# Performance work log

Measured on AMD Instinct MI355X. Metric: run time of the kernel, lower is better.

## Reference

```python
import jax, jax.numpy as jnp
import numpy as np

D_MODEL = 1024
H = 16
HEAD = D_MODEL // H  # 64


def setup_inputs() -> dict:
    key = jax.random.key(0)
    ks = jax.random.split(key, 10)
    B, S = 2, 2048
    x = jax.random.normal(ks[0], (B, S, D_MODEL), dtype=jnp.float32)
    y = jax.random.normal(ks[1], (B, S, D_MODEL), dtype=jnp.float32)
    mask = jnp.ones((B, S, S), dtype=jnp.float32)
    s = 1.0 / np.sqrt(D_MODEL)
    Wq = jax.random.normal(ks[2], (D_MODEL, D_MODEL), dtype=jnp.float32) * s
    Wk = jax.random.normal(ks[3], (D_MODEL, D_MODEL), dtype=jnp.float32) * s
    Wv = jax.random.normal(ks[4], (D_MODEL, D_MODEL), dtype=jnp.float32) * s
    Wo = jax.random.normal(ks[5], (D_MODEL, D_MODEL), dtype=jnp.float32) * s
    bq = jnp.zeros((D_MODEL,), jnp.float32)
    bk = jnp.zeros((D_MODEL,), jnp.float32)
    bv = jnp.zeros((D_MODEL,), jnp.float32)
    bo = jnp.zeros((D_MODEL,), jnp.float32)
    return {"x": x, "y": y, "mask": mask, "Wq": Wq, "bq": bq, "Wk": Wk,
            "bk": bk, "Wv": Wv, "bv": bv, "Wo": Wo, "bo": bo}


def reference(x, y, mask, Wq, bq, Wk, bk, Wv, bv, Wo, bo):
    # torch Linear: out = in @ W.T + b; here W stored as [out, in]
    B, Sq, D = x.shape
    Skv = y.shape[1]
    q = x @ Wq.T + bq  # [B, Sq, D]
    k = y @ Wk.T + bk  # [B, Skv, D]
    v = y @ Wv.T + bv
    # chunk(h, dim=-1) + cat(dim=0) == split feature dim into heads (head-major)
    q = q.reshape(B, Sq, H, HEAD)
    k = k.reshape(B, Skv, H, HEAD)
    v = v.reshape(B, Skv, H, HEAD)
    score = jnp.einsum('bqhd,bkhd->bhqk', q, k) / np.sqrt(HEAD)
    score = score + (1.0 - mask[:, None, :, :]) * -1e9
    attn = jax.nn.softmax(score, axis=-1)
    out = jnp.einsum('bhqk,bkhd->bqhd', attn, v).reshape(B, Sq, D)
    return out @ Wo.T + bo
```

## Files before the change

### kernel.cpp

```cpp
#include <hip/hip_runtime.h>
#include <cstdint>
#include <cstddef>

typedef __bf16 bf16x8 __attribute__((ext_vector_type(8)));
typedef float f32x4 __attribute__((ext_vector_type(4)));
typedef unsigned short u16;
typedef unsigned short u16x8 __attribute__((ext_vector_type(8)));
typedef unsigned int u32;

typedef __attribute__((address_space(1))) void gvoid_t;
typedef __attribute__((address_space(3))) void lvoid_t;

__device__ __forceinline__ void gld_lds16(const void* g, void* l) {
  __builtin_amdgcn_global_load_lds((gvoid_t*)g, (lvoid_t*)l, 16, 0, 0);
}

__device__ __forceinline__ u16 f2bf(float f) {
  u32 u = __float_as_uint(f);
  u += 0x7fffu + ((u >> 16) & 1u);
  return (u16)(u >> 16);
}
__device__ __forceinline__ u32 pack_rnd(float a, float b) {
  const u32 ua = __float_as_uint(a) + 0x8000u;
  const u32 ub = __float_as_uint(b) + 0x8000u;
  return __builtin_amdgcn_perm(ub, ua, 0x07060302u);
}
__device__ __forceinline__ bf16x8 ld_frag(const u16* p) {
  return __builtin_bit_cast(bf16x8, *(const uint4*)p);
}
__device__ __forceinline__ f32x4 mfma16(bf16x8 a, bf16x8 b, f32x4 c) {
  return __builtin_amdgcn_mfma_f32_16x16x32_bf16(a, b, c, 0, 0, 0);
}
__device__ __forceinline__ float ex2(float x) {
  return __builtin_amdgcn_exp2f(x);
}

#define D_MODEL 1024
#define SEQ     2048
#define NHEAD   16
#define QSC     0.1803368801f
#define MBIAS   (-1.4426950408e9f)

__global__ __launch_bounds__(256) void pre_kernel(
    const float* __restrict__ x,  const float* __restrict__ y,
    const float* __restrict__ wq, const float* __restrict__ wk,
    const float* __restrict__ wv,
    u16* __restrict__ xb, u16* __restrict__ yb,
    u16* __restrict__ wqb, u16* __restrict__ wkb,
    u16* __restrict__ wvb) {
  const int bid = blockIdx.x;
  const float* src;
  u16* dst;
  int base;
  float sA = 1.0f;
  if (bid < 2048)      { src = x;    dst = xb;    base = 0; }
  else if (bid < 4096) { src = y;    dst = yb;    base = 2048; }
  else if (bid < 4608) { src = wq;   dst = wqb;   base = 4096; sA = QSC; }
  else if (bid < 5120) { src = wk;   dst = wkb;   base = 4608; }
  else                 { src = wv;   dst = wvb;   base = 5120; }
  const int i = (((bid - base) * 256) + threadIdx.x) * 8;
  const float4 a = *(const float4*)(src + i);
  const float4 b = *(const float4*)(src + i + 4);
  ushort4 lo, hi;
  lo.x = f2bf(a.x * sA); lo.y = f2bf(a.y * sA);
  lo.z = f2bf(a.z * sA); lo.w = f2bf(a.w * sA);
  hi.x = f2bf(b.x * sA); hi.y = f2bf(b.y * sA);
  hi.z = f2bf(b.z * sA); hi.w = f2bf(b.w * sA);
  *(ushort4*)(dst + i) = lo;
  *(ushort4*)(dst + i + 4) = hi;
}

template <int MODE, typename OT>
__device__ __forceinline__ void gemm_block_128(u16* S,
                                               const u16* __restrict__ A,
                                               const u16* __restrict__ W,
                                               const float* __restrict__ bias,
                                               float bscale,
                                               OT* __restrict__ D,
                                               int mb, int nb) {
  u16* Asl = S;
  u16* Bsl = S + 8192;
  const int tid = threadIdx.x;
  const int w = tid >> 6, lane = tid & 63, quad = lane >> 4, l16 = lane & 15;
  const int wm = (w & 1) * 64, wn = (w >> 1) * 64;
  const int cidx = w * 64 + lane;

  f32x4 acc[4][4];
#pragma unroll
  for (int i = 0; i < 4; ++i)
#pragma unroll
    for (int j = 0; j < 4; ++j) acc[i][j] = f32x4{0.f, 0.f, 0.f, 0.f};

  for (int k0 = 0; k0 < 1024; k0 += 64) {
    __syncthreads();
#pragma unroll
    for (int t = 0; t < 4; ++t) {
      const int idx = t * 256 + cidx;
      const int row = idx >> 3;
      const int g = (idx & 7) ^ (row & 7);
      const size_t dst = (size_t)(t * 4 + w) * 1024;
      gld_lds16(A + (size_t)(mb * 128 + row) * 1024 + k0 + g * 8, (char*)Asl + dst);
      gld_lds16(W + (size_t)(nb * 128 + row) * 1024 + k0 + g * 8, (char*)Bsl + dst);
    }
    __syncthreads();

#pragma unroll
    for (int kk = 0; kk < 2; ++kk) {
      bf16x8 af[4], bfr[4];
#pragma unroll
      for (int i = 0; i < 4; ++i) {
        const int ar = wm + i * 16 + l16;
        const int br = wn + i * 16 + l16;
        af[i]  = ld_frag(Asl + ar * 64 + (((kk * 4 + quad) ^ (ar & 7)) * 8));
        bfr[i] = ld_frag(Bsl + br * 64 + (((kk * 4 + quad) ^ (br & 7)) * 8));
      }
#pragma unroll
      for (int i = 0; i < 4; ++i)
#pragma unroll
        for (int j = 0; j < 4; ++j) acc[i][j] = mfma16(af[i], bfr[j], acc[i][j]);
    }
  }

  if constexpr (MODE == 2) {
    __syncthreads();
#pragma unroll
    for (int i = 0; i < 4; ++i)
#pragma unroll
      for (int j = 0; j < 4; ++j) {
        const int dl = wn + j * 16 + l16;
        const float bv = bias[nb * 128 + dl];
        const int sx = (wm + i * 16 + quad * 4) ^ ((dl & 15) << 3);
        uint2 pv;
        pv.x = (u32)f2bf(acc[i][j][0] + bv) | ((u32)f2bf(acc[i][j][1] + bv) << 16);
        pv.y = (u32)f2bf(acc[i][j][2] + bv) | ((u32)f2bf(acc[i][j][3] + bv) << 16);
        *(uint2*)(S + dl * 128 + sx) = pv;
      }
    __syncthreads();
    const int dl = tid >> 1, half = tid & 1;
    const int bb = mb >> 4, s0 = (mb & 15) * 128;
    u16* vrow = (u16*)D + (size_t)(bb * 1024 + nb * 128 + dl) * SEQ + s0 + half * 64;
#pragma unroll
    for (int c = 0; c < 8; ++c) {
      const int pc = (half * 8 + c) ^ (dl & 15);
      *(uint4*)(vrow + c * 8) = *(const uint4*)(S + dl * 128 + pc * 8);
    }
  } else {
#pragma unroll
    for (int i = 0; i < 4; ++i)
#pragma unroll
      for (int j = 0; j < 4; ++j) {
        const int gn = nb * 128 + wn + j * 16 + l16;
        const float bv = bias[gn] * bscale;
#pragma unroll
        for (int r = 0; r < 4; ++r) {
          const int gm = mb * 128 + wm + i * 16 + quad * 4 + r;
          const float v = acc[i][j][r] + bv;
          if constexpr (sizeof(OT) == 2)
            D[(size_t)gm * 1024 + gn] = (OT)f2bf(v);
          else
            D[(size_t)gm * 1024 + gn] = (OT)v;
        }
      }
  }
}

__device__ __forceinline__ void gemm_block_n64(const u16* __restrict__ A,
                                               const u16* __restrict__ W,
                                               const float* __restrict__ bias,
                                               float* __restrict__ D,
                                               int mb, int nb) {
  __shared__ __align__(16) u16 S[12288];
  u16* Asl = S;
  u16* Bsl = S + 8192;
  const int tid = threadIdx.x;
  const int w = tid >> 6, lane = tid & 63, quad = lane >> 4, l16 = lane & 15;
  const int wm = w * 32;
  const int cidx = w * 64 + lane;

  f32x4 acc[2][4];
#pragma unroll
  for (int i = 0; i < 2; ++i)
#pragma unroll
    for (int j = 0; j < 4; ++j) acc[i][j] = f32x4{0.f, 0.f, 0.f, 0.f};

  for (int k0 = 0; k0 < 1024; k0 += 64) {
    __syncthreads();
#pragma unroll
    for (int t = 0; t < 4; ++t) {
      const int idx = t * 256 + cidx;
      const int row = idx >> 3;
      const int g = (idx & 7) ^ (row & 7);
      gld_lds16(A + (size_t)(mb * 128 + row) * 1024 + k0 + g * 8,
                (char*)Asl + (size_t)(t * 4 + w) * 1024);
    }
#pragma unroll
    for (int t = 0; t < 2; ++t) {
      const int idx = t * 256 + cidx;
      const int row = idx >> 3;
      const int g = (idx & 7) ^ (row & 7);
      gld_lds16(W + (size_t)(nb * 64 + row) * 1024 + k0 + g * 8,
                (char*)Bsl + (size_t)(t * 4 + w) * 1024);
    }
    __syncthreads();

#pragma unroll
    for (int kk = 0; kk < 2; ++kk) {
      bf16x8 af[2], bfr[4];
#pragma unroll
      for (int i = 0; i < 2; ++i) {
        const int ar = wm + i * 16 + l16;
        af[i] = ld_frag(Asl + ar * 64 + (((kk * 4 + quad) ^ (ar & 7)) * 8));
      }
#pragma unroll
      for (int j = 0; j < 4; ++j) {
        const int br = j * 16 + l16;
        bfr[j] = ld_frag(Bsl + br * 64 + (((kk * 4 + quad) ^ (br & 7)) * 8));
      }
#pragma unroll
      for (int i = 0; i < 2; ++i)
#pragma unroll
        for (int j = 0; j < 4; ++j) acc[i][j] = mfma16(af[i], bfr[j], acc[i][j]);
    }
  }

#pragma unroll
  for (int i = 0; i < 2; ++i)
#pragma unroll
    for (int j = 0; j < 4; ++j) {
      const int gn = nb * 64 + j * 16 + l16;
      const float bv = bias[gn];
#pragma unroll
      for (int r = 0; r < 4; ++r) {
        const int gm = mb * 128 + wm + i * 16 + quad * 4 + r;
        D[(size_t)gm * 1024 + gn] = acc[i][j][r] + bv;
      }
    }
}

__global__ __launch_bounds__(256) void qkv_kernel(
    const u16* __restrict__ xb, const u16* __restrict__ yb,
    const u16* __restrict__ Wqb, const u16* __restrict__ Wkb, const u16* __restrict__ Wvb,
    const float* __restrict__ bq, const float* __restrict__ bk, const float* __restrict__ bv,
    const float* __restrict__ mask, const float* __restrict__ wo,
    u16* __restrict__ qb, u16* __restrict__ kb, u16* __restrict__ vt,
    u16* __restrict__ wob, u32* __restrict__ flags) {
  __shared__ __align__(16) u16 S[16384];
  const int by = blockIdx.y;
  if (by < 4) {
    const int mx = by * 32 + blockIdx.x;
    const int lane = threadIdx.x & 63, wv8 = threadIdx.x >> 6;
    for (int r = 0; r < 32; ++r) {
      const int row = mx * 32 + r;
      const size_t i = (size_t)row * SEQ + threadIdx.x * 8;
      const float4 a = *(const float4*)(mask + i);
      const float4 b = *(const float4*)(mask + i + 4);
      const bool m8 = (a.x != 1.f) || (a.y != 1.f) || (a.z != 1.f) || (a.w != 1.f) ||
                      (b.x != 1.f) || (b.y != 1.f) || (b.z != 1.f) || (b.w != 1.f);
      const unsigned long long bal = __ballot(m8);
      if (lane == 0) {
        u32 bits = 0;
#pragma unroll
        for (int g = 0; g < 8; ++g)
          bits |= (((bal >> (8 * g)) & 0xFFull) ? 1u : 0u) << g;
        if (bits) {
          const int bb = row >> 11, q = row & 2047;
          atomicOr(&flags[bb * 32 + (q >> 6)], bits << (wv8 * 8));
        }
      }
    }
    return;
  }
  if (by < 20) {
    const int wid = (by - 4) * 32 + blockIdx.x;
    const int i = (wid * 256 + threadIdx.x) * 8;
    const float4 a = *(const float4*)(wo + i);
    const float4 b = *(const float4*)(wo + i + 4);
    ushort4 lo, hi;
    lo.x = f2bf(a.x); lo.y = f2bf(a.y); lo.z = f2bf(a.z); lo.w = f2bf(a.w);
    hi.x = f2bf(b.x); hi.y = f2bf(b.y); hi.z = f2bf(b.z); hi.w = f2bf(b.w);
    *(ushort4*)(wob + i) = lo;
    *(ushort4*)(wob + i + 4) = hi;
    return;
  }
  const int mat = (by - 20) >> 3;
  const int nb = (by - 20) & 7;
  const int mb = blockIdx.x;
  if (mat == 0)      gemm_block_128<0, u16>(S, xb, Wqb, bq, QSC,  qb, mb, nb);
  else if (mat == 1) gemm_block_128<0, u16>(S, yb, Wkb, bk, 1.0f, kb, mb, nb);
  else               gemm_block_128<2, u16>(S, yb, Wvb, bv, 1.0f, vt, mb, nb);
}

__global__ __launch_bounds__(256) void oproj_kernel(
    const u16* __restrict__ ctx, const u16* __restrict__ Wob,
    const float* __restrict__ bo, float* __restrict__ out) {
  gemm_block_n64(ctx, Wob, bo, out, blockIdx.x, blockIdx.y);
}

__global__ __launch_bounds__(256, 4) void attn_kernel(
    const u16* __restrict__ qb, const u16* __restrict__ kb,
    const u16* __restrict__ vt, const float* __restrict__ mask,
    const u32* __restrict__ flags, u16* __restrict__ ctx) {
  const int h = blockIdx.x;
  const int qblk = blockIdx.y;
  const int b = blockIdx.z;
  const int tid = threadIdx.x, w = tid >> 6, lane = tid & 63;
  const int quad = lane >> 4, l16 = lane & 15;
  const int q0 = qblk * 64;

  __shared__ __align__(16) u16 Ks[64 * 64];
  __shared__ __align__(16) u16 Vs[64 * 64];
  __shared__ __align__(16) u16 Ps[64 * 64];

  const u32 fl = flags[(b << 5) + qblk];

  const int qrow = w * 16 + l16;
  const u16* qp = qb + (size_t)(b * SEQ + q0 + qrow) * D_MODEL + h * 64;
  const bf16x8 qf0 = ld_frag(qp + quad * 8);
  const bf16x8 qf1 = ld_frag(qp + 32 + quad * 8);

  bf16x8 onesf;
  {
    u16x8 t;
    const u16 ov = (l16 == 0) ? (u16)0x3F80 : (u16)0;
#pragma unroll
    for (int j = 0; j < 8; ++j) t[j] = ov;
    onesf = __builtin_bit_cast(bf16x8, t);
  }

  f32x4 O[4];
#pragma unroll
  for (int dt = 0; dt < 4; ++dt) O[dt] = f32x4{0.f, 0.f, 0.f, 0.f};
  f32x4 O4 = f32x4{0.f, 0.f, 0.f, 0.f};

  const int cidx = w * 64 + lane;
  const int bhalf = (quad & 1) * 4;

  const u16 *kf0p[4], *kf1p[4], *vf0p[4], *vf1p[4];
  u16* psp[4];
#pragma unroll
  for (int nt = 0; nt < 4; ++nt) {
    const int rl = nt * 16 + l16;
    kf0p[nt] = Ks + rl * 64 + ((quad ^ (rl & 7)) * 8);
    kf1p[nt] = Ks + rl * 64 + (((4 + quad) ^ (rl & 7)) * 8);
    vf0p[nt] = Vs + rl * 64 + ((quad ^ (rl & 7)) * 8);
    vf1p[nt] = Vs + rl * 64 + (((4 + quad) ^ (rl & 7)) * 8);
    const int ck = nt * 2 + (quad >> 1);
    psp[nt] = Ps + qrow * 64 + ((ck ^ (qrow & 7)) * 8) + bhalf;
  }
  const u16* pf0p = Ps + qrow * 64 + ((quad ^ (qrow & 7)) * 8);
  const u16* pf1p = Ps + qrow * 64 + (((4 + quad) ^ (qrow & 7)) * 8);

  const int r0 = cidx >> 3,        g0 = (cidx & 7) ^ (r0 & 7);
  const int r1 = (256 + cidx) >> 3, g1 = ((256 + cidx) & 7) ^ (r1 & 7);
  const u16* kp0 = kb + (size_t)(b * SEQ + r0) * D_MODEL + h * 64 + g0 * 8;
  const u16* kp1 = kb + (size_t)(b * SEQ + r1) * D_MODEL + h * 64 + g1 * 8;
  const u16* vp0 = vt + ((size_t)((b * NHEAD + h) * 64 + r0)) * SEQ + g0 * 8;
  const u16* vp1 = vt + ((size_t)((b * NHEAD + h) * 64 + r1)) * SEQ + g1 * 8;
  const float* mp = mask + (size_t)(b * SEQ + q0 + qrow) * SEQ + quad * 4;
  const size_t dst0 = (size_t)w * 1024;
  const size_t dst1 = (size_t)(4 + w) * 1024;

  for (int kt = 0; kt < 32; ++kt) {
    const bool doBias = (fl >> kt) & 1u;
    __syncthreads();
    gld_lds16(kp0, (char*)Ks + dst0);
    gld_lds16(kp1, (char*)Ks + dst1);
    gld_lds16(vp0, (char*)Vs + dst0);
    gld_lds16(vp1, (char*)Vs + dst1);
    kp0 += 64 * D_MODEL; kp1 += 64 * D_MODEL;
    vp0 += 64;           vp1 += 64;
    __syncthreads();

    f32x4 z[4];
    __builtin_amdgcn_s_setprio(1);
#pragma unroll
    for (int nt = 0; nt < 4; ++nt) {
      const bf16x8 kf0 = ld_frag(kf0p[nt]);
      const bf16x8 kf1 = ld_frag(kf1p[nt]);
      f32x4 zz;
      if (doBias) {
        const float4 mv = *(const float4*)(mp + nt * 16);
        zz[0] = (1.f - mv.x) * MBIAS;
        zz[1] = (1.f - mv.y) * MBIAS;
        zz[2] = (1.f - mv.z) * MBIAS;
        zz[3] = (1.f - mv.w) * MBIAS;
      } else {
        zz = f32x4{0.f, 0.f, 0.f, 0.f};
      }
      zz = mfma16(kf0, qf0, zz);
      zz = mfma16(kf1, qf1, zz);
      z[nt] = zz;
    }
    __builtin_amdgcn_s_setprio(0);
    mp += 64;
#pragma unroll
    for (int nt = 0; nt < 4; ++nt) {
      uint2 pv;
      pv.x = pack_rnd(ex2(z[nt][0]), ex2(z[nt][1]));
      pv.y = pack_rnd(ex2(z[nt][2]), ex2(z[nt][3]));
      *(uint2*)psp[nt] = pv;
    }

    const bf16x8 pf0 = ld_frag(pf0p);
    const bf16x8 pf1 = ld_frag(pf1p);
    __builtin_amdgcn_s_setprio(1);
#pragma unroll
    for (int dt = 0; dt < 4; ++dt) {
      const bf16x8 vf0 = ld_frag(vf0p[dt]);
      const bf16x8 vf1 = ld_frag(vf1p[dt]);
      O[dt] = mfma16(pf0, vf0, O[dt]);
      O[dt] = mfma16(pf1, vf1, O[dt]);
    }
    O4 = mfma16(pf0, onesf, O4);
    O4 = mfma16(pf1, onesf, O4);
    __builtin_amdgcn_s_setprio(0);
  }

  float inv[4];
#pragma unroll
  for (int r = 0; r < 4; ++r)
    inv[r] = 1.0f / __shfl(O4[r], lane & 48, 64);

#pragma unroll
  for (int dt = 0; dt < 4; ++dt)
#pragma unroll
    for (int r = 0; r < 4; ++r) {
      const int gq = b * SEQ + q0 + w * 16 + quad * 4 + r;
      const int gd = h * 64 + dt * 16 + l16;
      ctx[(size_t)gq * D_MODEL + gd] = f2bf(O[dt][r] * inv[r]);
    }
}

extern "C" void kernel_launch(void* const* d_in, const int* in_sizes, int n_in,
                              void* d_out, int out_size, void* d_ws, size_t ws_size,
                              hipStream_t stream) {
  (void)in_sizes; (void)n_in; (void)out_size; (void)ws_size;
  const float* x    = (const float*)d_in[0];
  const float* y    = (const float*)d_in[1];
  const float* mask = (const float*)d_in[2];
  const float* Wq   = (const float*)d_in[3];
  const float* bq   = (const float*)d_in[4];
  const float* Wk   = (const float*)d_in[5];
  const float* bk   = (const float*)d_in[6];
  const float* Wv   = (const float*)d_in[7];
  const float* bv   = (const float*)d_in[8];
  const float* Wo   = (const float*)d_in[9];
  const float* bo   = (const float*)d_in[10];
  float* out = (float*)d_out;

  const size_t M4 = (size_t)4096 * 1024;
  const size_t M1 = (size_t)1024 * 1024;
  u16* qbuf  = (u16*)d_ws;
  u16* kbuf  = qbuf + M4;
  u16* vt    = kbuf + M4;
  u16* cbuf  = vt + M4;
  u16* wob   = cbuf + M4;
  u16* xb    = wob + M1;
  u16* yb    = xb + M4;
  u16* wqb   = yb + M4;
  u16* wkb   = wqb + M1;
  u16* wvb   = wkb + M1;
  u32* flags = (u32*)(wvb + M1);

  hipMemsetAsync(flags, 0, 64 * sizeof(u32), stream);
  pre_kernel<<<dim3(5632, 1, 1), 256, 0, stream>>>(
      x, y, Wq, Wk, Wv, xb, yb, wqb, wkb, wvb);
  qkv_kernel<<<dim3(32, 44, 1), 256, 0, stream>>>(xb, yb, wqb, wkb, wvb,
                                                  bq, bk, bv, mask, Wo,
                                                  qbuf, kbuf, vt, wob, flags);
  attn_kernel<<<dim3(NHEAD, 32, 2), 256, 0, stream>>>(qbuf, kbuf, vt, mask, flags, cbuf);
  oproj_kernel<<<dim3(32, 16, 1), 256, 0, stream>>>(cbuf, wob, bo, out);
}
```

Measured before the change: 238.9 us.

## Split attention warps 2x2 over query and key halves with LDS reduction

Changes the per-block warp work split in the attention kernel. Before, each of the four warps owned 16 query rows across all 64 keys. Now the warps form a 2x2 grid: each owns 32 query rows and half of the key tile, so each K and V fragment loaded from LDS is reused across two query subtiles. The per-warp partial O and row sums are combined at the end through LDS. This adds a final barrier, more registers per thread, and an epilogue where half the warps sit idle.

```diff
diff --git a/kernel.cpp b/kernel.cpp
--- a/kernel.cpp
+++ b/kernel.cpp
@@ -305,6 +305,7 @@
   const int b = blockIdx.z;
   const int tid = threadIdx.x, w = tid >> 6, lane = tid & 63;
   const int quad = lane >> 4, l16 = lane & 15;
+  const int qg = w & 1, kg = w >> 1;
   const int q0 = qblk * 64;
 
   __shared__ __align__(16) u16 Ks[64 * 64];
@@ -313,10 +314,14 @@
 
   const u32 fl = flags[(b << 5) + qblk];
 
-  const int qrow = w * 16 + l16;
-  const u16* qp = qb + (size_t)(b * SEQ + q0 + qrow) * D_MODEL + h * 64;
-  const bf16x8 qf0 = ld_frag(qp + quad * 8);
-  const bf16x8 qf1 = ld_frag(qp + 32 + quad * 8);
+  bf16x8 qf[2][2];
+#pragma unroll
+  for (int qs = 0; qs < 2; ++qs) {
+    const int qrow = qg * 32 + qs * 16 + l16;
+    const u16* qp = qb + (size_t)(b * SEQ + q0 + qrow) * D_MODEL + h * 64;
+    qf[qs][0] = ld_frag(qp + quad * 8);
+    qf[qs][1] = ld_frag(qp + 32 + quad * 8);
+  }
 
   bf16x8 onesf;
   {
@@ -327,28 +332,39 @@
     onesf = __builtin_bit_cast(bf16x8, t);
   }
 
-  f32x4 O[4];
-#pragma unroll
-  for (int dt = 0; dt < 4; ++dt) O[dt] = f32x4{0.f, 0.f, 0.f, 0.f};
-  f32x4 O4 = f32x4{0.f, 0.f, 0.f, 0.f};
+  f32x4 O[4][2];
+#pragma unroll
+  for (int dt = 0; dt < 4; ++dt)
+#pragma unroll
+    for (int qs = 0; qs < 2; ++qs) O[dt][qs] = f32x4{0.f, 0.f, 0.f, 0.f};
+  f32x4 L[2] = {f32x4{0.f, 0.f, 0.f, 0.f}, f32x4{0.f, 0.f, 0.f, 0.f}};
 
   const int cidx = w * 64 + lane;
   const int bhalf = (quad & 1) * 4;
 
-  const u16 *kf0p[4], *kf1p[4], *vf0p[4], *vf1p[4];
-  u16* psp[4];
-#pragma unroll
-  for (int nt = 0; nt < 4; ++nt) {
-    const int rl = nt * 16 + l16;
-    kf0p[nt] = Ks + rl * 64 + ((quad ^ (rl & 7)) * 8);
-    kf1p[nt] = Ks + rl * 64 + (((4 + quad) ^ (rl & 7)) * 8);
-    vf0p[nt] = Vs + rl * 64 + ((quad ^ (rl & 7)) * 8);
-    vf1p[nt] = Vs + rl * 64 + (((4 + quad) ^ (rl & 7)) * 8);
-    const int ck = nt * 2 + (quad >> 1);
-    psp[nt] = Ps + qrow * 64 + ((ck ^ (qrow & 7)) * 8) + bhalf;
-  }
-  const u16* pf0p = Ps + qrow * 64 + ((quad ^ (qrow & 7)) * 8);
-  const u16* pf1p = Ps + qrow * 64 + (((4 + quad) ^ (qrow & 7)) * 8);
+  const u16 *kf0p[2], *kf1p[2], *vfp[4], *pfp[2];
+  u16* psp[2][2];
+#pragma unroll
+  for (int nt = 0; nt < 2; ++nt) {
+    const int kvl = kg * 32 + nt * 16 + l16;
+    kf0p[nt] = Ks + kvl * 64 + ((quad ^ (kvl & 7)) * 8);
+    kf1p[nt] = Ks + kvl * 64 + (((4 + quad) ^ (kvl & 7)) * 8);
+  }
+#pragma unroll
+  for (int dt = 0; dt < 4; ++dt) {
+    const int vr = dt * 16 + l16;
+    vfp[dt] = Vs + vr * 64 + ((((kg * 4) + quad) ^ (vr & 7)) * 8);
+  }
+#pragma unroll
+  for (int qs = 0; qs < 2; ++qs) {
+    const int prow = qg * 32 + qs * 16 + l16;
+    pfp[qs] = Ps + prow * 64 + ((((kg * 4) + quad) ^ (prow & 7)) * 8);
+#pragma unroll
+    for (int nt = 0; nt < 2; ++nt) {
+      const int ck = kg * 4 + nt * 2 + (quad >> 1);
+      psp[qs][nt] = Ps + prow * 64 + ((ck ^ (prow & 7)) * 8) + bhalf;
+    }
+  }
 
   const int r0 = cidx >> 3,        g0 = (cidx & 7) ^ (r0 & 7);
   const int r1 = (256 + cidx) >> 3, g1 = ((256 + cidx) & 7) ^ (r1 & 7);
@@ -356,7 +372,11 @@
   const u16* kp1 = kb + (size_t)(b * SEQ + r1) * D_MODEL + h * 64 + g1 * 8;
   const u16* vp0 = vt + ((size_t)((b * NHEAD + h) * 64 + r0)) * SEQ + g0 * 8;
   const u16* vp1 = vt + ((size_t)((b * NHEAD + h) * 64 + r1)) * SEQ + g1 * 8;
-  const float* mp = mask + (size_t)(b * SEQ + q0 + qrow) * SEQ + quad * 4;
+  const float* mp[2];
+#pragma unroll
+  for (int qs = 0; qs < 2; ++qs)
+    mp[qs] = mask + (size_t)(b * SEQ + q0 + qg * 32 + qs * 16 + l16) * SEQ
+                  + kg * 32 + quad * 4;
   const size_t dst0 = (size_t)w * 1024;
   const size_t dst1 = (size_t)(4 + w) * 1024;
 
@@ -371,64 +391,102 @@
     vp0 += 64;           vp1 += 64;
     __syncthreads();
 
-    f32x4 z[4];
+    f32x4 z[2][2];
     __builtin_amdgcn_s_setprio(1);
 #pragma unroll
-    for (int nt = 0; nt < 4; ++nt) {
+    for (int nt = 0; nt < 2; ++nt) {
       const bf16x8 kf0 = ld_frag(kf0p[nt]);
       const bf16x8 kf1 = ld_frag(kf1p[nt]);
-      f32x4 zz;
-      if (doBias) {
-        const float4 mv = *(const float4*)(mp + nt * 16);
-        zz[0] = (1.f - mv.x) * MBIAS;
-        zz[1] = (1.f - mv.y) * MBIAS;
-        zz[2] = (1.f - mv.z) * MBIAS;
-        zz[3] = (1.f - mv.w) * MBIAS;
-      } else {
-        zz = f32x4{0.f, 0.f, 0.f, 0.f};
-      }
-      zz = mfma16(kf0, qf0, zz);
-      zz = mfma16(kf1, qf1, zz);
-      z[nt] = zz;
+#pragma unroll
+      for (int qs = 0; qs < 2; ++qs) {
+        f32x4 zz;
+        if (doBias) {
+          const float4 mv = *(const float4*)(mp[qs] + nt * 16);
+          zz[0] = (1.f - mv.x) * MBIAS;
+          zz[1] = (1.f - mv.y) * MBIAS;
+          zz[2] = (1.f - mv.z) * MBIAS;
+          zz[3] = (1.f - mv.w) * MBIAS;
+        } else {
+          zz = f32x4{0.f, 0.f, 0.f, 0.f};
+        }
+        zz = mfma16(kf0, qf[qs][0], zz);
+        zz = mfma16(kf1, qf[qs][1], zz);
+        z[nt][qs] = zz;
+      }
     }
     __builtin_amdgcn_s_setprio(0);
-    mp += 64;
-#pragma unroll
-    for (int nt = 0; nt < 4; ++nt) {
-      uint2 pv;
-      pv.x = pack_rnd(ex2(z[nt][0]), ex2(z[nt][1]));
-      pv.y = pack_rnd(ex2(z[nt][2]), ex2(z[nt][3]));
-      *(uint2*)psp[nt] = pv;
-    }
-
-    const bf16x8 pf0 = ld_frag(pf0p);
-    const bf16x8 pf1 = ld_frag(pf1p);
+    mp[0] += 64; mp[1] += 64;
+
+#pragma unroll
+    for (int nt = 0; nt < 2; ++nt)
+#pragma unroll
+      for (int qs = 0; qs < 2; ++qs) {
+        uint2 pv;
+        pv.x = pack_rnd(ex2(z[nt][qs][0]), ex2(z[nt][qs][1]));
+        pv.y = pack_rnd(ex2(z[nt][qs][2]), ex2(z[nt][qs][3]));
+        *(uint2*)psp[qs][nt] = pv;
+      }
+
+    const bf16x8 pf0 = ld_frag(pfp[0]);
+    const bf16x8 pf1 = ld_frag(pfp[1]);
     __builtin_amdgcn_s_setprio(1);
 #pragma unroll
     for (int dt = 0; dt < 4; ++dt) {
-      const bf16x8 vf0 = ld_frag(vf0p[dt]);
-      const bf16x8 vf1 = ld_frag(vf1p[dt]);
-      O[dt] = mfma16(pf0, vf0, O[dt]);
-      O[dt] = mfma16(pf1, vf1, O[dt]);
-    }
-    O4 = mfma16(pf0, onesf, O4);
-    O4 = mfma16(pf1, onesf, O4);
+      const bf16x8 vf = ld_frag(vfp[dt]);
+      O[dt][0] = mfma16(pf0, vf, O[dt][0]);
+      O[dt][1] = mfma16(pf1, vf, O[dt][1]);
+    }
+    L[0] = mfma16(pf0, onesf, L[0]);
+    L[1] = mfma16(pf1, onesf, L[1]);
     __builtin_amdgcn_s_setprio(0);
   }
 
-  float inv[4];
-#pragma unroll
-  for (int r = 0; r < 4; ++r)
-    inv[r] = 1.0f / __shfl(O4[r], lane & 48, 64);
-
-#pragma unroll
-  for (int dt = 0; dt < 4; ++dt)
-#pragma unroll
-    for (int r = 0; r < 4; ++r) {
-      const int gq = b * SEQ + q0 + w * 16 + quad * 4 + r;
-      const int gd = h * 64 + dt * 16 + l16;
-      ctx[(size_t)gq * D_MODEL + gd] = f2bf(O[dt][r] * inv[r]);
-    }
+  __syncthreads();
+  {
+    float* Of = (float*)(qg ? Vs : Ks);
+    float* Lf = (float*)Ps;
+    if (kg == 1) {
+#pragma unroll
+      for (int dt = 0; dt < 4; ++dt)
+#pragma unroll
+        for (int qs = 0; qs < 2; ++qs)
+          *(f32x4*)(Of + (qs * 4 + dt) * 256 + lane * 4) = O[dt][qs];
+#pragma unroll
+      for (int qs = 0; qs < 2; ++qs)
+        *(f32x4*)(Lf + (qg * 2 + qs) * 256 + lane * 4) = L[qs];
+    }
+  }
+  __syncthreads();
+  if (kg == 0) {
+    const float* Of = (const float*)(qg ? Vs : Ks);
+    const float* Lf = (const float*)Ps;
+#pragma unroll
+    for (int dt = 0; dt < 4; ++dt)
+#pragma unroll
+      for (int qs = 0; qs < 2; ++qs)
+        O[dt][qs] += *(const f32x4*)(Of + (qs * 4 + dt) * 256 + lane * 4);
+#pragma unroll
+    for (int qs = 0; qs < 2; ++qs)
+      L[qs] += *(const f32x4*)(Lf + (qg * 2 + qs) * 256 + lane * 4);
+
+    float inv[2][4];
+#pragma unroll
+    for (int qs = 0; qs < 2; ++qs)
+#pragma unroll
+      for (int r = 0; r < 4; ++r)
+        inv[qs][r] = 1.0f / __shfl(L[qs][r], lane & 48, 64);
+
+#pragma unroll
+    for (int dt = 0; dt < 4; ++dt)
+#pragma unroll
+      for (int qs = 0; qs < 2; ++qs)
+#pragma unroll
+        for (int r = 0; r < 4; ++r) {
+          const int gq = b * SEQ + q0 + qg * 32 + qs * 16 + quad * 4 + r;
+          const int gd = h * 64 + dt * 16 + l16;
+          ctx[(size_t)gq * D_MODEL + gd] = f2bf(O[dt][qs][r] * inv[qs][r]);
+        }
+  }
 }
 
 extern "C" void kernel_launch(void* const* d_in, const int* in_sizes, int n_in,
```

After: 239.2 us. About the same (+0.1%).

## Split attention KV tile across warp pairs with 32-row query blocks

Applied to the files above, without the earlier changes.

Each attention block now handles 32 query rows instead of 64. Its four warps are arranged as 2 query groups by 2 key halves, and each warp computes scores and PV for half of the 64-key tile. Partial O and row sums are reduced through shared memory at the end. The grid doubles and launch bounds are raised so more blocks fit per CU, at the cost of loading each K/V tile twice as often per query row and an extra reduction step.

```diff
diff --git a/kernel.cpp b/kernel.cpp
--- a/kernel.cpp
+++ b/kernel.cpp
@@ -296,7 +296,7 @@
   gemm_block_n64(ctx, Wob, bo, out, blockIdx.x, blockIdx.y);
 }
 
-__global__ __launch_bounds__(256, 4) void attn_kernel(
+__global__ __launch_bounds__(256, 8) void attn_kernel(
     const u16* __restrict__ qb, const u16* __restrict__ kb,
     const u16* __restrict__ vt, const float* __restrict__ mask,
     const u32* __restrict__ flags, u16* __restrict__ ctx) {
@@ -305,15 +305,16 @@
   const int b = blockIdx.z;
   const int tid = threadIdx.x, w = tid >> 6, lane = tid & 63;
   const int quad = lane >> 4, l16 = lane & 15;
-  const int q0 = qblk * 64;
+  const int qg = w & 1, kg = w >> 1;
+  const int q0 = qblk * 32;
 
   __shared__ __align__(16) u16 Ks[64 * 64];
   __shared__ __align__(16) u16 Vs[64 * 64];
-  __shared__ __align__(16) u16 Ps[64 * 64];
-
-  const u32 fl = flags[(b << 5) + qblk];
-
-  const int qrow = w * 16 + l16;
+  __shared__ __align__(16) u16 Ps[32 * 64];
+
+  const u32 fl = flags[(b << 5) + (qblk >> 1)];
+
+  const int qrow = qg * 16 + l16;
   const u16* qp = qb + (size_t)(b * SEQ + q0 + qrow) * D_MODEL + h * 64;
   const bf16x8 qf0 = ld_frag(qp + quad * 8);
   const bf16x8 qf1 = ld_frag(qp + 32 + quad * 8);
@@ -330,25 +331,33 @@
   f32x4 O[4];
 #pragma unroll
   for (int dt = 0; dt < 4; ++dt) O[dt] = f32x4{0.f, 0.f, 0.f, 0.f};
-  f32x4 O4 = f32x4{0.f, 0.f, 0.f, 0.f};
+  f32x4 L = f32x4{0.f, 0.f, 0.f, 0.f};
 
   const int cidx = w * 64 + lane;
   const int bhalf = (quad & 1) * 4;
 
-  const u16 *kf0p[4], *kf1p[4], *vf0p[4], *vf1p[4];
-  u16* psp[4];
-#pragma unroll
-  for (int nt = 0; nt < 4; ++nt) {
-    const int rl = nt * 16 + l16;
-    kf0p[nt] = Ks + rl * 64 + ((quad ^ (rl & 7)) * 8);
-    kf1p[nt] = Ks + rl * 64 + (((4 + quad) ^ (rl & 7)) * 8);
-    vf0p[nt] = Vs + rl * 64 + ((quad ^ (rl & 7)) * 8);
-    vf1p[nt] = Vs + rl * 64 + (((4 + quad) ^ (rl & 7)) * 8);
-    const int ck = nt * 2 + (quad >> 1);
-    psp[nt] = Ps + qrow * 64 + ((ck ^ (qrow & 7)) * 8) + bhalf;
-  }
-  const u16* pf0p = Ps + qrow * 64 + ((quad ^ (qrow & 7)) * 8);
-  const u16* pf1p = Ps + qrow * 64 + (((4 + quad) ^ (qrow & 7)) * 8);
+  const u16 *kf0p[2], *kf1p[2], *vfp[4], *pfp;
+  u16* psp[2];
+#pragma unroll
+  for (int nt = 0; nt < 2; ++nt) {
+    const int kvl = kg * 32 + nt * 16 + l16;
+    kf0p[nt] = Ks + kvl * 64 + ((quad ^ (kvl & 7)) * 8);
+    kf1p[nt] = Ks + kvl * 64 + (((4 + quad) ^ (kvl & 7)) * 8);
+  }
+#pragma unroll
+  for (int dt = 0; dt < 4; ++dt) {
+    const int vr = dt * 16 + l16;
+    vfp[dt] = Vs + vr * 64 + ((((kg * 4) + quad) ^ (vr & 7)) * 8);
+  }
+  {
+    const int prow = qg * 16 + l16;
+    pfp = Ps + prow * 64 + ((((kg * 4) + quad) ^ (prow & 7)) * 8);
+#pragma unroll
+    for (int nt = 0; nt < 2; ++nt) {
+      const int ck = kg * 4 + nt * 2 + (quad >> 1);
+      psp[nt] = Ps + prow * 64 + ((ck ^ (prow & 7)) * 8) + bhalf;
+    }
+  }
 
   const int r0 = cidx >> 3,        g0 = (cidx & 7) ^ (r0 & 7);
   const int r1 = (256 + cidx) >> 3, g1 = ((256 + cidx) & 7) ^ (r1 & 7);
@@ -356,7 +365,7 @@
   const u16* kp1 = kb + (size_t)(b * SEQ + r1) * D_MODEL + h * 64 + g1 * 8;
   const u16* vp0 = vt + ((size_t)((b * NHEAD + h) * 64 + r0)) * SEQ + g0 * 8;
   const u16* vp1 = vt + ((size_t)((b * NHEAD + h) * 64 + r1)) * SEQ + g1 * 8;
-  const float* mp = mask + (size_t)(b * SEQ + q0 + qrow) * SEQ + quad * 4;
+  const float* mp = mask + (size_t)(b * SEQ + q0 + qrow) * SEQ + kg * 32 + quad * 4;
   const size_t dst0 = (size_t)w * 1024;
   const size_t dst1 = (size_t)(4 + w) * 1024;
 
@@ -371,10 +380,10 @@
     vp0 += 64;           vp1 += 64;
     __syncthreads();
 
-    f32x4 z[4];
+    f32x4 z[2];
     __builtin_amdgcn_s_setprio(1);
 #pragma unroll
-    for (int nt = 0; nt < 4; ++nt) {
+    for (int nt = 0; nt < 2; ++nt) {
       const bf16x8 kf0 = ld_frag(kf0p[nt]);
       const bf16x8 kf1 = ld_frag(kf1p[nt]);
       f32x4 zz;
@@ -393,42 +402,58 @@
     }
     __builtin_amdgcn_s_setprio(0);
     mp += 64;
-#pragma unroll
-    for (int nt = 0; nt < 4; ++nt) {
+
+#pragma unroll
+    for (int nt = 0; nt < 2; ++nt) {
       uint2 pv;
       pv.x = pack_rnd(ex2(z[nt][0]), ex2(z[nt][1]));
       pv.y = pack_rnd(ex2(z[nt][2]), ex2(z[nt][3]));
       *(uint2*)psp[nt] = pv;
     }
 
-    const bf16x8 pf0 = ld_frag(pf0p);
-    const bf16x8 pf1 = ld_frag(pf1p);
+    const bf16x8 pf = ld_frag(pfp);
     __builtin_amdgcn_s_setprio(1);
 #pragma unroll
     for (int dt = 0; dt < 4; ++dt) {
-      const bf16x8 vf0 = ld_frag(vf0p[dt]);
-      const bf16x8 vf1 = ld_frag(vf1p[dt]);
-      O[dt] = mfma16(pf0, vf0, O[dt]);
-      O[dt] = mfma16(pf1, vf1, O[dt]);
-    }
-    O4 = mfma16(pf0, onesf, O4);
-    O4 = mfma16(pf1, onesf, O4);
+      const bf16x8 vf = ld_frag(vfp[dt]);
+      O[dt] = mfma16(pf, vf, O[dt]);
+    }
+    L = mfma16(pf, onesf, L);
     __builtin_amdgcn_s_setprio(0);
   }
 
-  float inv[4];
-#pragma unroll
-  for (int r = 0; r < 4; ++r)
-    inv[r] = 1.0f / __shfl(O4[r], lane & 48, 64);
-
-#pragma unroll
-  for (int dt = 0; dt < 4; ++dt)
-#pragma unroll
-    for (int r = 0; r < 4; ++r) {
-      const int gq = b * SEQ + q0 + w * 16 + quad * 4 + r;
-      const int gd = h * 64 + dt * 16 + l16;
-      ctx[(size_t)gq * D_MODEL + gd] = f2bf(O[dt][r] * inv[r]);
-    }
+  __syncthreads();
+  if (kg == 1) {
+    float* Of = (float*)(qg ? Vs : Ks);
+    float* Lf = (float*)Ps + qg * 256;
+#pragma unroll
+    for (int dt = 0; dt < 4; ++dt)
+      *(f32x4*)(Of + dt * 256 + lane * 4) = O[dt];
+    *(f32x4*)(Lf + lane * 4) = L;
+  }
+  __syncthreads();
+  if (kg == 0) {
+    const float* Of = (const float*)(qg ? Vs : Ks);
+    const float* Lf = (const float*)Ps + qg * 256;
+#pragma unroll
+    for (int dt = 0; dt < 4; ++dt)
+      O[dt] += *(const f32x4*)(Of + dt * 256 + lane * 4);
+    L += *(const f32x4*)(Lf + lane * 4);
+
+    float inv[4];
+#pragma unroll
+    for (int r = 0; r < 4; ++r)
+      inv[r] = 1.0f / __shfl(L[r], lane & 48, 64);
+
+#pragma unroll
+    for (int dt = 0; dt < 4; ++dt)
+#pragma unroll
+      for (int r = 0; r < 4; ++r) {
+        const int gq = b * SEQ + q0 + qg * 16 + quad * 4 + r;
+        const int gd = h * 64 + dt * 16 + l16;
+        ctx[(size_t)gq * D_MODEL + gd] = f2bf(O[dt][r] * inv[r]);
+      }
+  }
 }
 
 extern "C" void kernel_launch(void* const* d_in, const int* in_sizes, int n_in,
@@ -468,6 +493,6 @@
   qkv_kernel<<<dim3(32, 44, 1), 256, 0, stream>>>(xb, yb, wqb, wkb, wvb,
                                                   bq, bk, bv, mask, Wo,
                                                   qbuf, kbuf, vt, wob, flags);
-  attn_kernel<<<dim3(NHEAD, 32, 2), 256, 0, stream>>>(qbuf, kbuf, vt, mask, flags, cbuf);
+  attn_kernel<<<dim3(NHEAD, 64, 2), 256, 0, stream>>>(qbuf, kbuf, vt, mask, flags, cbuf);
   oproj_kernel<<<dim3(32, 16, 1), 256, 0, stream>>>(cbuf, wob, bo, out);
 }
```

Result: slower. 262.5 us (+9.9%).

## Fuse all stages into one persistent cooperative kernel with grid syncs

Applied to the files above, without the earlier changes.

Merges the memset, conversion, QKV GEMM, mask scan, attention and output projection into a single cooperative launch. Persistent blocks walk a work index and use grid-wide barriers between phases. This removes per-kernel launch gaps and the separate memset. In exchange, every stage now shares one launch-bounds and register budget, and the 32KB of shared memory per block may limit occupancy. The attention and o-proj phases are also capped by the persistent grid size, and grid barriers add their own cost.

```diff
diff --git a/kernel.cpp b/kernel.cpp
--- a/kernel.cpp
+++ b/kernel.cpp
@@ -1,6 +1,9 @@
 #include <hip/hip_runtime.h>
+#include <hip/hip_cooperative_groups.h>
 #include <cstdint>
 #include <cstddef>
+
+namespace cg = cooperative_groups;
 
 typedef __bf16 bf16x8 __attribute__((ext_vector_type(8)));
 typedef float f32x4 __attribute__((ext_vector_type(4)));
@@ -40,35 +43,6 @@
 #define NHEAD   16
 #define QSC     0.1803368801f
 #define MBIAS   (-1.4426950408e9f)
-
-__global__ __launch_bounds__(256) void pre_kernel(
-    const float* __restrict__ x,  const float* __restrict__ y,
-    const float* __restrict__ wq, const float* __restrict__ wk,
-    const float* __restrict__ wv,
-    u16* __restrict__ xb, u16* __restrict__ yb,
-    u16* __restrict__ wqb, u16* __restrict__ wkb,
-    u16* __restrict__ wvb) {
-  const int bid = blockIdx.x;
-  const float* src;
-  u16* dst;
-  int base;
-  float sA = 1.0f;
-  if (bid < 2048)      { src = x;    dst = xb;    base = 0; }
-  else if (bid < 4096) { src = y;    dst = yb;    base = 2048; }
-  else if (bid < 4608) { src = wq;   dst = wqb;   base = 4096; sA = QSC; }
-  else if (bid < 5120) { src = wk;   dst = wkb;   base = 4608; }
-  else                 { src = wv;   dst = wvb;   base = 5120; }
-  const int i = (((bid - base) * 256) + threadIdx.x) * 8;
-  const float4 a = *(const float4*)(src + i);
-  const float4 b = *(const float4*)(src + i + 4);
-  ushort4 lo, hi;
-  lo.x = f2bf(a.x * sA); lo.y = f2bf(a.y * sA);
-  lo.z = f2bf(a.z * sA); lo.w = f2bf(a.w * sA);
-  hi.x = f2bf(b.x * sA); hi.y = f2bf(b.y * sA);
-  hi.z = f2bf(b.z * sA); hi.w = f2bf(b.w * sA);
-  *(ushort4*)(dst + i) = lo;
-  *(ushort4*)(dst + i + 4) = hi;
-}
 
 template <int MODE, typename OT>
 __device__ __forceinline__ void gemm_block_128(u16* S,
@@ -164,12 +138,12 @@
   }
 }
 
-__device__ __forceinline__ void gemm_block_n64(const u16* __restrict__ A,
+__device__ __forceinline__ void gemm_block_n64(u16* S,
+                                               const u16* __restrict__ A,
                                                const u16* __restrict__ W,
                                                const float* __restrict__ bias,
                                                float* __restrict__ D,
                                                int mb, int nb) {
-  __shared__ __align__(16) u16 S[12288];
   u16* Asl = S;
   u16* Bsl = S + 8192;
   const int tid = threadIdx.x;
@@ -237,79 +211,20 @@
     }
 }
 
-__global__ __launch_bounds__(256) void qkv_kernel(
-    const u16* __restrict__ xb, const u16* __restrict__ yb,
-    const u16* __restrict__ Wqb, const u16* __restrict__ Wkb, const u16* __restrict__ Wvb,
-    const float* __restrict__ bq, const float* __restrict__ bk, const float* __restrict__ bv,
-    const float* __restrict__ mask, const float* __restrict__ wo,
-    u16* __restrict__ qb, u16* __restrict__ kb, u16* __restrict__ vt,
-    u16* __restrict__ wob, u32* __restrict__ flags) {
-  __shared__ __align__(16) u16 S[16384];
-  const int by = blockIdx.y;
-  if (by < 4) {
-    const int mx = by * 32 + blockIdx.x;
-    const int lane = threadIdx.x & 63, wv8 = threadIdx.x >> 6;
-    for (int r = 0; r < 32; ++r) {
-      const int row = mx * 32 + r;
-      const size_t i = (size_t)row * SEQ + threadIdx.x * 8;
-      const float4 a = *(const float4*)(mask + i);
-      const float4 b = *(const float4*)(mask + i + 4);
-      const bool m8 = (a.x != 1.f) || (a.y != 1.f) || (a.z != 1.f) || (a.w != 1.f) ||
-                      (b.x != 1.f) || (b.y != 1.f) || (b.z != 1.f) || (b.w != 1.f);
-      const unsigned long long bal = __ballot(m8);
-      if (lane == 0) {
-        u32 bits = 0;
-#pragma unroll
-        for (int g = 0; g < 8; ++g)
-          bits |= (((bal >> (8 * g)) & 0xFFull) ? 1u : 0u) << g;
-        if (bits) {
-          const int bb = row >> 11, q = row & 2047;
-          atomicOr(&flags[bb * 32 + (q >> 6)], bits << (wv8 * 8));
-        }
-      }
-    }
-    return;
-  }
-  if (by < 20) {
-    const int wid = (by - 4) * 32 + blockIdx.x;
-    const int i = (wid * 256 + threadIdx.x) * 8;
-    const float4 a = *(const float4*)(wo + i);
-    const float4 b = *(const float4*)(wo + i + 4);
-    ushort4 lo, hi;
-    lo.x = f2bf(a.x); lo.y = f2bf(a.y); lo.z = f2bf(a.z); lo.w = f2bf(a.w);
-    hi.x = f2bf(b.x); hi.y = f2bf(b.y); hi.z = f2bf(b.z); hi.w = f2bf(b.w);
-    *(ushort4*)(wob + i) = lo;
-    *(ushort4*)(wob + i + 4) = hi;
-    return;
-  }
-  const int mat = (by - 20) >> 3;
-  const int nb = (by - 20) & 7;
-  const int mb = blockIdx.x;
-  if (mat == 0)      gemm_block_128<0, u16>(S, xb, Wqb, bq, QSC,  qb, mb, nb);
-  else if (mat == 1) gemm_block_128<0, u16>(S, yb, Wkb, bk, 1.0f, kb, mb, nb);
-  else               gemm_block_128<2, u16>(S, yb, Wvb, bv, 1.0f, vt, mb, nb);
-}
-
-__global__ __launch_bounds__(256) void oproj_kernel(
-    const u16* __restrict__ ctx, const u16* __restrict__ Wob,
-    const float* __restrict__ bo, float* __restrict__ out) {
-  gemm_block_n64(ctx, Wob, bo, out, blockIdx.x, blockIdx.y);
-}
-
-__global__ __launch_bounds__(256, 4) void attn_kernel(
+__device__ __forceinline__ void attn_block(
+    u16* S, int u,
     const u16* __restrict__ qb, const u16* __restrict__ kb,
     const u16* __restrict__ vt, const float* __restrict__ mask,
     const u32* __restrict__ flags, u16* __restrict__ ctx) {
-  const int h = blockIdx.x;
-  const int qblk = blockIdx.y;
-  const int b = blockIdx.z;
+  const int h = u & 15;
+  const int qblk = (u >> 4) & 31;
+  const int b = u >> 9;
+  u16* Ks = S;
+  u16* Vs = S + 4096;
+  u16* Ps = S + 8192;
   const int tid = threadIdx.x, w = tid >> 6, lane = tid & 63;
   const int quad = lane >> 4, l16 = lane & 15;
   const int q0 = qblk * 64;
-
-  __shared__ __align__(16) u16 Ks[64 * 64];
-  __shared__ __align__(16) u16 Vs[64 * 64];
-  __shared__ __align__(16) u16 Ps[64 * 64];
 
   const u32 fl = flags[(b << 5) + qblk];
 
@@ -429,6 +344,94 @@
       const int gd = h * 64 + dt * 16 + l16;
       ctx[(size_t)gq * D_MODEL + gd] = f2bf(O[dt][r] * inv[r]);
     }
+}
+
+__global__ __launch_bounds__(256, 4) void fused_kernel(
+    const float* __restrict__ x,  const float* __restrict__ y,
+    const float* __restrict__ mask,
+    const float* __restrict__ wq, const float* __restrict__ wk,
+    const float* __restrict__ wv, const float* __restrict__ wo,
+    const float* __restrict__ bq, const float* __restrict__ bk,
+    const float* __restrict__ bv, const float* __restrict__ bo,
+    u16* __restrict__ xb, u16* __restrict__ yb,
+    u16* __restrict__ wqb, u16* __restrict__ wkb, u16* __restrict__ wvb,
+    u16* __restrict__ wob,
+    u16* __restrict__ qbuf, u16* __restrict__ kbuf, u16* __restrict__ vt,
+    u16* __restrict__ cbuf, u32* __restrict__ flags,
+    float* __restrict__ out) {
+  __shared__ __align__(16) u16 S[16384];
+  cg::grid_group grid = cg::this_grid();
+  const u32 nbk = gridDim.x;
+
+  if (blockIdx.x == 0 && threadIdx.x < 64) flags[threadIdx.x] = 0;
+  for (u32 u = blockIdx.x; u < 5632; u += nbk) {
+    const float* src; u16* dst; u32 base; float sA = 1.0f;
+    if (u < 2048)      { src = x;  dst = xb;  base = 0; }
+    else if (u < 4096) { src = y;  dst = yb;  base = 2048; }
+    else if (u < 4608) { src = wq; dst = wqb; base = 4096; sA = QSC; }
+    else if (u < 5120) { src = wk; dst = wkb; base = 4608; }
+    else               { src = wv; dst = wvb; base = 5120; }
+    const int i = (int)((u - base) * 256 + threadIdx.x) * 8;
+    const float4 a = *(const float4*)(src + i);
+    const float4 b4 = *(const float4*)(src + i + 4);
+    ushort4 lo, hi;
+    lo.x = f2bf(a.x * sA);  lo.y = f2bf(a.y * sA);
+    lo.z = f2bf(a.z * sA);  lo.w = f2bf(a.w * sA);
+    hi.x = f2bf(b4.x * sA); hi.y = f2bf(b4.y * sA);
+    hi.z = f2bf(b4.z * sA); hi.w = f2bf(b4.w * sA);
+    *(ushort4*)(dst + i) = lo;
+    *(ushort4*)(dst + i + 4) = hi;
+  }
+  grid.sync();
+
+  for (u32 u = blockIdx.x; u < 1408; u += nbk) {
+    if (u < 768) {
+      const int mat = u >> 8, rest = u & 255, nbq = rest >> 5, mb = rest & 31;
+      if (mat == 0)      gemm_block_128<0, u16>(S, xb, wqb, bq, QSC,  qbuf, mb, nbq);
+      else if (mat == 1) gemm_block_128<0, u16>(S, yb, wkb, bk, 1.0f, kbuf, mb, nbq);
+      else               gemm_block_128<2, u16>(S, yb, wvb, bv, 1.0f, vt,   mb, nbq);
+    } else if (u < 896) {
+      const int mx = u - 768;
+      const int lane = threadIdx.x & 63, wv8 = threadIdx.x >> 6;
+      for (int r = 0; r < 32; ++r) {
+        const int row = mx * 32 + r;
+        const size_t i = (size_t)row * SEQ + threadIdx.x * 8;
+        const float4 a = *(const float4*)(mask + i);
+        const float4 b4 = *(const float4*)(mask + i + 4);
+        const bool m8 = (a.x != 1.f) || (a.y != 1.f) || (a.z != 1.f) || (a.w != 1.f) ||
+                        (b4.x != 1.f) || (b4.y != 1.f) || (b4.z != 1.f) || (b4.w != 1.f);
+        const unsigned long long bal = __ballot(m8);
+        if (lane == 0) {
+          u32 bits = 0;
+#pragma unroll
+          for (int g = 0; g < 8; ++g)
+            bits |= (((bal >> (8 * g)) & 0xFFull) ? 1u : 0u) << g;
+          if (bits) {
+            const int bb = row >> 11, q = row & 2047;
+            atomicOr(&flags[bb * 32 + (q >> 6)], bits << (wv8 * 8));
+          }
+        }
+      }
+    } else {
+      const int wid = u - 896;
+      const int i = (wid * 256 + threadIdx.x) * 8;
+      const float4 a = *(const float4*)(wo + i);
+      const float4 b4 = *(const float4*)(wo + i + 4);
+      ushort4 lo, hi;
+      lo.x = f2bf(a.x);  lo.y = f2bf(a.y);  lo.z = f2bf(a.z);  lo.w = f2bf(a.w);
+      hi.x = f2bf(b4.x); hi.y = f2bf(b4.y); hi.z = f2bf(b4.z); hi.w = f2bf(b4.w);
+      *(ushort4*)(wob + i) = lo;
+      *(ushort4*)(wob + i + 4) = hi;
+    }
+  }
+  grid.sync();
+
+  for (u32 u = blockIdx.x; u < 1024; u += nbk)
+    attn_block(S, (int)u, qbuf, kbuf, vt, mask, flags, cbuf);
+  grid.sync();
+
+  for (u32 u = blockIdx.x; u < 512; u += nbk)
+    gemm_block_n64(S, cbuf, wob, bo, out, (int)(u & 31), (int)(u >> 5));
 }
 
 extern "C" void kernel_launch(void* const* d_in, const int* in_sizes, int n_in,
@@ -462,12 +465,23 @@
   u16* wvb   = wkb + M1;
   u32* flags = (u32*)(wvb + M1);
 
-  hipMemsetAsync(flags, 0, 64 * sizeof(u32), stream);
-  pre_kernel<<<dim3(5632, 1, 1), 256, 0, stream>>>(
-      x, y, Wq, Wk, Wv, xb, yb, wqb, wkb, wvb);
-  qkv_kernel<<<dim3(32, 44, 1), 256, 0, stream>>>(xb, yb, wqb, wkb, wvb,
-                                                  bq, bk, bv, mask, Wo,
-                                                  qbuf, kbuf, vt, wob, flags);
-  attn_kernel<<<dim3(NHEAD, 32, 2), 256, 0, stream>>>(qbuf, kbuf, vt, mask, flags, cbuf);
-  oproj_kernel<<<dim3(32, 16, 1), 256, 0, stream>>>(cbuf, wob, bo, out);
-}
+  static int gridSz = 0;
+  if (gridSz == 0) {
+    int mpb = 0;
+    hipOccupancyMaxActiveBlocksPerMultiprocessor(&mpb, fused_kernel, 256, 0);
+    if (mpb < 1) mpb = 1;
+    long cap = (long)mpb * 256;
+    gridSz = (int)(cap < 1024 ? cap : 1024);
+  }
+
+  void* args[] = {
+      (void*)&x, (void*)&y, (void*)&mask,
+      (void*)&Wq, (void*)&Wk, (void*)&Wv, (void*)&Wo,
+      (void*)&bq, (void*)&bk, (void*)&bv, (void*)&bo,
+      (void*)&xb, (void*)&yb, (void*)&wqb, (void*)&wkb, (void*)&wvb,
+      (void*)&wob,
+      (void*)&qbuf, (void*)&kbuf, (void*)&vt, (void*)&cbuf, (void*)&flags,
+      (void*)&out};
+  hipLaunchCooperativeKernel((const void*)fused_kernel, dim3(gridSz),
+                             dim3(256), args, 0, stream);
+}
```

After: 486.3 us. 104% more time.
